# Performance work log

Hardware: AMD Instinct MI355X
Metric: run time of the kernel (lower is better)

Reference implementation:

```python
import jax, jax.numpy as jnp
import numpy as np

PAD = 1
ORDERS = ['back', 'down', 'front', 'left', 'right', 'top']
# connected face for each of ['up','down','left','right'] sides (from self.relation)
NEIGHBORS = {
    'back':  ['top', 'down', 'right', 'left'],
    'down':  ['front', 'back', 'left', 'right'],
    'front': ['top', 'down', 'left', 'right'],
    'left':  ['top', 'down', 'back', 'front'],
    'right': ['top', 'down', 'front', 'back'],
    'top':   ['back', 'front', 'left', 'right'],
}
SIDES = ['up', 'down', 'left', 'right']

def _rot_y(t):
    c, s = np.cos(t), np.sin(t)
    return np.array([[c, 0, s], [0, 1, 0], [-s, 0, c]], np.float64)

def _rot_x(t):
    c, s = np.cos(t), np.sin(t)
    return np.array([[1, 0, 0], [0, c, -s], [0, s, c]], np.float64)

def _precompute(h, pad):
    # Reconstruction of Equirec2Cube geometry used by SpherePad._GetLoc.
    # Padded cube face has side Wp = h + 2*pad and FOV theta = 2*arctan((0.5h+pad)/(0.5h)).
    Wp = h + 2 * pad
    cxp = (Wp - 1) / 2.0
    tan_half = (0.5 * h + pad) / (0.5 * h)  # tan(theta/2)
    fp = cxp / tan_half                      # focal of padded cube (pixel-edge convention)
    u = (np.arange(Wp) - cxp) / fp
    gx, gy = np.meshgrid(u, u)              # x right, y down, camera looks along +z
    grid = np.stack([gx, gy, np.ones_like(gx)], axis=-1)  # [Wp, Wp, 3] front-face rays
    # world->camera rotations per face, ordered/named to match ORDERS
    R = {'back': _rot_y(np.pi), 'down': _rot_x(np.pi / 2), 'front': np.eye(3),
         'left': _rot_y(np.pi / 2), 'right': _rot_y(-np.pi / 2), 'top': _rot_x(-np.pi / 2)}
    data = {}
    for face in ORDERS:
        data[face] = {}
        for j, side in enumerate(SIDES):
            conn = NEIGHBORS[face][j]
            Rrel = R[conn] @ R[face].T       # self-cam -> connected-cam
            g = grid @ Rrel.T                # [Wp, Wp, 3]
            # original FOV=90 K has f == cx, so normalized grid_sample coord = X/Z, Y/Z
            x = g[..., 0] / g[..., 2]
            y = g[..., 1] / g[..., 2]
            mask = (x >= -1.01) & (x <= 1.01) & (y >= -1.01) & (y <= 1.01)
            xy = np.clip(np.stack([x, y], axis=-1), -1.0, 1.0).astype(np.float32)
            if side == 'up':
                sl = (slice(0, pad), slice(None))
            elif side == 'down':
                sl = (slice(Wp - pad, Wp), slice(None))
            elif side == 'left':
                sl = (slice(None), slice(0, pad))
            else:
                sl = (slice(None), slice(Wp - pad, Wp))
            data[face][side] = (xy[sl], mask[sl])
    return data

def _grid_sample(img, grid):
    # img [N,C,H,W], grid [N,Hg,Wg,2] in [-1,1]; bilinear, align_corners=True
    N, C, H, W = img.shape
    x = (grid[..., 0] + 1.0) * 0.5 * (W - 1)
    y = (grid[..., 1] + 1.0) * 0.5 * (H - 1)
    x0 = jnp.floor(x)
    y0 = jnp.floor(y)
    wx = (x - x0)[..., None]
    wy = (y - y0)[..., None]
    x0i = jnp.clip(x0.astype(jnp.int32), 0, W - 1)
    x1i = jnp.clip(x0i + 1, 0, W - 1)
    y0i = jnp.clip(y0.astype(jnp.int32), 0, H - 1)
    y1i = jnp.clip(y0i + 1, 0, H - 1)
    b = jnp.arange(N)[:, None, None]
    v00 = img[b, :, y0i, x0i]  # [N,Hg,Wg,C]
    v01 = img[b, :, y0i, x1i]
    v10 = img[b, :, y1i, x0i]
    v11 = img[b, :, y1i, x1i]
    out = (v00 * (1 - wx) * (1 - wy) + v01 * wx * (1 - wy)
           + v10 * (1 - wx) * wy + v11 * wx * wy)
    return out.transpose(0, 3, 1, 2)  # [N,C,Hg,Wg]

def _forward(inputs, pad):
    bs, c, h, w = inputs.shape
    rep = bs // 6
    data = _precompute(h, pad)       # numpy constants, computed at trace time
    faces = inputs.reshape(rep, 6, c, h, w)   # inputs[i::6] == faces[:, i]
    outs = []
    for i, face in enumerate(ORDERS):
        tf = jnp.pad(faces[:, i], ((0, 0), (0, 0), (pad, pad), (pad, pad)))
        for j, side in enumerate(SIDES):
            conn = faces[:, ORDERS.index(NEIGHBORS[face][j])]
            xy, mask = data[face][side]
            grid = jnp.broadcast_to(jnp.asarray(xy), (rep,) + xy.shape)
            interp = _grid_sample(conn, grid)          # [rep,c,strip_h,strip_w]
            m = jnp.asarray(mask)[None, None]
            if side == 'up':
                tf = tf.at[:, :, :pad, :].set(jnp.where(m, interp, tf[:, :, :pad, :]))
            elif side == 'down':
                tf = tf.at[:, :, -pad:, :].set(jnp.where(m, interp, tf[:, :, -pad:, :]))
            elif side == 'left':
                tf = tf.at[:, :, :, :pad].set(jnp.where(m, interp, tf[:, :, :, :pad]))
            else:
                tf = tf.at[:, :, :, -pad:].set(jnp.where(m, interp, tf[:, :, :, -pad:]))
        outs.append(tf)
    # torch: cat by face then re-interleave -> out[k*6+i] = face i of panorama k
    return jnp.stack(outs, axis=1).reshape(bs, c, h + 2 * pad, w + 2 * pad)

def setup_inputs() -> dict:
    key = jax.random.key(0)
    inputs = jax.random.normal(key, (24, 256, 128, 128), dtype=jnp.float32)
    return {'inputs': inputs}

def reference(inputs):
    return _forward(inputs, PAD)
```

## Files before the change

kernel.cpp:

```cpp
#include <hip/hip_runtime.h>

#define H    128
#define WP   130
#define BPF  516
#define TBLN 3096

__constant__ int c_R[6][9] = {
  {-1,0,0,  0,1,0,  0,0,-1},
  { 1,0,0,  0,0,-1, 0,1,0 },
  { 1,0,0,  0,1,0,  0,0,1 },
  { 0,0,1,  0,1,0, -1,0,0 },
  { 0,0,-1, 0,1,0,  1,0,0 },
  { 1,0,0,  0,0,1,  0,-1,0},
};
__constant__ int c_conn[6][4] = {
  {5,1,4,3}, {2,0,3,4}, {5,1,3,4}, {5,1,0,2}, {5,1,2,0}, {0,2,3,4},
};

#define INV_FP (65.0f / 4128.0f)

__global__ void __launch_bounds__(256)
border_table_kernel(int* __restrict__ tb_face, int4* __restrict__ tb_idx,
                    float4* __restrict__ tb_w) {
  int t = blockIdx.x * 256 + threadIdx.x;
  if (t >= TBLN) return;
  int face = t / BPF;
  int k    = t - face * BPF;

  int r, c;
  if (k < 130)      { r = 0;        c = k; }
  else if (k < 260) { r = WP - 1;   c = k - 130; }
  else if (k < 388) { r = k - 259;  c = 0; }
  else              { r = k - 387;  c = WP - 1; }

  int fs = -1;
  int4  idx = make_int4(0, 0, 0, 0);
  float4 w  = make_float4(0.f, 0.f, 0.f, 0.f);

  int cand[2]; int nc = 0;
  if (c == WP - 1) cand[nc++] = 3;
  if (c == 0)      cand[nc++] = 2;
  if (r == WP - 1) cand[nc++] = 1;
  if (r == 0)      cand[nc++] = 0;

  float uc = ((float)c - 64.5f) * INV_FP;
  float ur = ((float)r - 64.5f) * INV_FP;

  for (int kk = 0; kk < nc; ++kk) {
    int s  = cand[kk];
    int cf = c_conn[face][s];
    const int* Rc = c_R[cf];
    const int* Rf = c_R[face];
    float g[3];
    #pragma unroll
    for (int i = 0; i < 3; ++i) {
      float acc = 0.0f;
      #pragma unroll
      for (int j = 0; j < 3; ++j) {
        int rr = Rc[i*3+0]*Rf[j*3+0] + Rc[i*3+1]*Rf[j*3+1] + Rc[i*3+2]*Rf[j*3+2];
        float dj = (j == 0) ? uc : (j == 1) ? ur : 1.0f;
        acc += (float)rr * dj;
      }
      g[i] = acc;
    }
    float x = g[0] / g[2];
    float y = g[1] / g[2];
    if (fabsf(x) <= 1.01f && fabsf(y) <= 1.01f) {
      x = fminf(fmaxf(x, -1.0f), 1.0f);
      y = fminf(fmaxf(y, -1.0f), 1.0f);
      float xp = (x + 1.0f) * 0.5f * (float)(H - 1);
      float yp = (y + 1.0f) * 0.5f * (float)(H - 1);
      float x0 = floorf(xp), y0 = floorf(yp);
      float wx = xp - x0,    wy = yp - y0;
      int x0i = min(max((int)x0, 0), H - 1);
      int x1i = min(x0i + 1, H - 1);
      int y0i = min(max((int)y0, 0), H - 1);
      int y1i = min(y0i + 1, H - 1);
      fs  = cf;
      idx = make_int4(y0i * H + x0i, y0i * H + x1i, y1i * H + x0i, y1i * H + x1i);
      w   = make_float4((1.f - wx) * (1.f - wy), wx * (1.f - wy),
                        (1.f - wx) * wy,         wx * wy);
      break;
    }
  }
  tb_face[t] = fs;
  tb_idx[t]  = idx;
  tb_w[t]    = w;
}

__global__ void __launch_bounds__(256)
fused_kernel(const float* __restrict__ in, float4* __restrict__ out4,
             const int* __restrict__ tb_face,
             const int4* __restrict__ tb_idx,
             const float4* __restrict__ tb_w) {
  const unsigned bx  = blockIdx.x;
  const unsigned img = blockIdx.y;
  const unsigned u   = threadIdx.x;

  if (bx < 16u) {
    unsigned hh = (bx << 3) + (u >> 5);
    unsigned l  = u & 31u;
    unsigned g  = hh + 1u;
    unsigned m  = g >> 1;
    unsigned h  = g & 1u;

    const float4* base = (const float4*)in + ((size_t)img << 12);
    float4 A = base[(hh << 5) + l];
    float bx0 = __shfl_down(A.x, 1, 32);
    float by0 = __shfl_down(A.y, 1, 32);
    float bz0 = __shfl_down(A.z, 1, 32);

    float4 o = h ? make_float4(A.y, A.z, A.w, bx0)
                 : make_float4(A.w, bx0, by0, bz0);
    if (l < 31u)
      out4[(size_t)img * 4225u + 65u * m + 1u + (h << 5) + l] = o;
  } else {
    unsigned n    = img >> 8;
    unsigned ch   = img & 255u;
    unsigned rep  = n / 6u;
    unsigned face = n - rep * 6u;

    for (unsigned k = u; k < 257u; k += 256u) {
      unsigned qk;
      if (k < 33u)       qk = k;
      else if (k == 33u) qk = 64u;
      else if (k == 34u) qk = 4160u;
      else if (k < 68u)  qk = 4192u + (k - 35u);
      else {
        unsigned jj = k - 68u;
        unsigned mm = 1u + jj / 3u;
        unsigned w  = jj - 3u * (jj / 3u);
        qk = 65u * mm + ((w == 0u) ? 0u : (w == 1u) ? 32u : 64u);
      }

      unsigned p = qk << 2;
      unsigned r = p / 130u;
      unsigned c = p - r * 130u;
      float vals[4];
      #pragma unroll
      for (int jj = 0; jj < 4; ++jj) {
        float v;
        if ((r - 1u) < 128u && (c - 1u) < 128u) {
          v = in[(img << 14) + ((r - 1u) << 7) + (c - 1u)];
        } else {
          unsigned tk = (r == 0u)   ? c
                      : (r == 129u) ? (130u + c)
                      : (c == 0u)   ? (259u + r)
                      :               (387u + r);
          unsigned ti = face * (unsigned)BPF + tk;
          int fs = tb_face[ti];
          v = 0.0f;
          if (fs >= 0) {
            int4   id = tb_idx[ti];
            float4 w  = tb_w[ti];
            const float* s = in +
                ((size_t)(((rep * 6u + (unsigned)fs) << 8) + ch) << 14);
            v = w.x * s[id.x] + w.y * s[id.y] + w.z * s[id.z] + w.w * s[id.w];
          }
        }
        vals[jj] = v;
        if (++c == 130u) { c = 0u; ++r; }
      }
      out4[(size_t)img * 4225u + qk] =
          make_float4(vals[0], vals[1], vals[2], vals[3]);
    }
  }
}

__global__ void __launch_bounds__(256)
interior_kernel(const float4* __restrict__ in4, float* __restrict__ out) {
  unsigned t = blockIdx.x * 256u + threadIdx.x;
  unsigned c4  = t & 31u;
  unsigned r   = (t >> 5) & 127u;
  unsigned img = t >> 12;
  float4 v = in4[t];
  unsigned o = img * 16900u + (r + 1u) * 130u + 1u + (c4 << 2);
  out[o] = v.x; out[o + 1] = v.y; out[o + 2] = v.z; out[o + 3] = v.w;
}

__global__ void __launch_bounds__(256)
border_kernel(const float* __restrict__ in, float* __restrict__ out) {
  unsigned tid = blockIdx.x * 256u + threadIdx.x;
  const unsigned total = 6144u * 516u;
  if (tid >= total) return;
  unsigned img = tid / 516u;
  unsigned k   = tid - img * 516u;
  int r, c;
  if (k < 130u)      { r = 0;               c = (int)k; }
  else if (k < 260u) { r = WP - 1;          c = (int)(k - 130u); }
  else if (k < 388u) { r = (int)(k - 259u); c = 0; }
  else               { r = (int)(k - 387u); c = WP - 1; }
  int n = (int)(img >> 8), ch = (int)(img & 255u);
  int face = n % 6, rep = n / 6;
  float v = 0.0f;
  int cand[2]; int nc = 0;
  if (c == WP - 1) cand[nc++] = 3;
  if (c == 0)      cand[nc++] = 2;
  if (r == WP - 1) cand[nc++] = 1;
  if (r == 0)      cand[nc++] = 0;
  float uc = ((float)c - 64.5f) * INV_FP;
  float ur = ((float)r - 64.5f) * INV_FP;
  for (int kk = 0; kk < nc; ++kk) {
    int s = cand[kk], cf = c_conn[face][s];
    const int* Rc = c_R[cf]; const int* Rf = c_R[face];
    float g[3];
    #pragma unroll
    for (int i = 0; i < 3; ++i) {
      float acc = 0.0f;
      #pragma unroll
      for (int j = 0; j < 3; ++j) {
        int rr = Rc[i*3+0]*Rf[j*3+0] + Rc[i*3+1]*Rf[j*3+1] + Rc[i*3+2]*Rf[j*3+2];
        float dj = (j == 0) ? uc : (j == 1) ? ur : 1.0f;
        acc += (float)rr * dj;
      }
      g[i] = acc;
    }
    float x = g[0] / g[2], y = g[1] / g[2];
    if (fabsf(x) <= 1.01f && fabsf(y) <= 1.01f) {
      x = fminf(fmaxf(x, -1.0f), 1.0f);
      y = fminf(fmaxf(y, -1.0f), 1.0f);
      const float* src = in + ((size_t)((rep * 6 + cf) * 256 + ch)) * H * H;
      float xp = (x + 1.0f) * 0.5f * (float)(H - 1);
      float yp = (y + 1.0f) * 0.5f * (float)(H - 1);
      float x0 = floorf(xp), y0 = floorf(yp);
      float wx = xp - x0, wy = yp - y0;
      int x0i = min(max((int)x0, 0), H - 1);
      int x1i = min(x0i + 1, H - 1);
      int y0i = min(max((int)y0, 0), H - 1);
      int y1i = min(y0i + 1, H - 1);
      v = src[y0i*H+x0i]*(1.f-wx)*(1.f-wy) + src[y0i*H+x1i]*wx*(1.f-wy)
        + src[y1i*H+x0i]*(1.f-wx)*wy       + src[y1i*H+x1i]*wx*wy;
      break;
    }
  }
  out[(unsigned)img * 16900u + (unsigned)r * 130u + (unsigned)c] = v;
}

extern "C" void kernel_launch(void* const* d_in, const int* in_sizes, int n_in,
                              void* d_out, int out_size, void* d_ws, size_t ws_size,
                              hipStream_t stream) {
  (void)in_sizes; (void)n_in; (void)out_size;
  const float* in = (const float*)d_in[0];
  float* out = (float*)d_out;

  const size_t need = (size_t)TBLN * (4 + 16 + 16);
  if (d_ws != nullptr && ws_size >= need) {
    int*    tb_face = (int*)d_ws;
    int4*   tb_idx  = (int4*)(tb_face + TBLN);
    float4* tb_w    = (float4*)(tb_idx + TBLN);
    border_table_kernel<<<(TBLN + 255) / 256, 256, 0, stream>>>(tb_face, tb_idx, tb_w);

    dim3 grid(17, 6144);
    fused_kernel<<<grid, 256, 0, stream>>>(in, (float4*)out,
                                           tb_face, tb_idx, tb_w);
  } else {
    interior_kernel<<<98304, 256, 0, stream>>>((const float4*)in, out);
    const unsigned btotal = 6144u * 516u;
    border_kernel<<<(btotal + 255u) / 256u, 256, 0, stream>>>(in, out);
  }
}
```

Baseline: 240.8 us.

## Stage image edge rows/columns in workspace so border pass reads compact buffer

The bulk copy kernel now also writes each image's first/last two rows and first/last four columns into a compact per-image staging buffer in workspace. A separate edge kernel then computes the border strips and bilinear samples from this staged data, using precomputed staged indices, instead of gathering scattered values from the full input. This aims to turn strided, poorly coalesced border gathers into reads from a small contiguous region. In exchange it adds an extra kernel launch, a dependency between the two passes, and about 37 MB of staging writes and reads.

```diff
diff --git a/kernel.cpp b/kernel.cpp
--- a/kernel.cpp
+++ b/kernel.cpp
@@ -4,6 +4,7 @@
 #define WP   130
 #define BPF  516
 #define TBLN 3096
+#define SPI  1536
 
 __constant__ int c_R[6][9] = {
   {-1,0,0,  0,1,0,  0,0,-1},
@@ -19,9 +20,16 @@
 
 #define INV_FP (65.0f / 4128.0f)
 
-__global__ void __launch_bounds__(256)
-border_table_kernel(int* __restrict__ tb_face, int4* __restrict__ tb_idx,
-                    float4* __restrict__ tb_w) {
+__device__ __forceinline__ int stage_index(int y, int x) {
+  if (x <= 3)   return 512 + y * 8 + x;
+  if (x >= 124) return 512 + y * 8 + 4 + (x - 124);
+  int slot = (y == 0) ? 0 : (y == 1) ? 1 : (y == 126) ? 2 : 3;
+  return slot * 128 + x;
+}
+
+__global__ void __launch_bounds__(256)
+border_table_kernel(int* __restrict__ tb_face, int4* __restrict__ tb_raw,
+                    int4* __restrict__ tb_stg, float4* __restrict__ tb_w) {
   int t = blockIdx.x * 256 + threadIdx.x;
   if (t >= TBLN) return;
   int face = t / BPF;
@@ -34,7 +42,8 @@
   else              { r = k - 387;  c = WP - 1; }
 
   int fs = -1;
-  int4  idx = make_int4(0, 0, 0, 0);
+  int4  raw = make_int4(0, 0, 0, 0);
+  int4  stg = make_int4(0, 0, 0, 0);
   float4 w  = make_float4(0.f, 0.f, 0.f, 0.f);
 
   int cand[2]; int nc = 0;
@@ -77,15 +86,113 @@
       int y0i = min(max((int)y0, 0), H - 1);
       int y1i = min(y0i + 1, H - 1);
       fs  = cf;
-      idx = make_int4(y0i * H + x0i, y0i * H + x1i, y1i * H + x0i, y1i * H + x1i);
+      raw = make_int4(y0i * H + x0i, y0i * H + x1i, y1i * H + x0i, y1i * H + x1i);
+      stg = make_int4(stage_index(y0i, x0i), stage_index(y0i, x1i),
+                      stage_index(y1i, x0i), stage_index(y1i, x1i));
       w   = make_float4((1.f - wx) * (1.f - wy), wx * (1.f - wy),
                         (1.f - wx) * wy,         wx * wy);
       break;
     }
   }
   tb_face[t] = fs;
-  tb_idx[t]  = idx;
+  tb_raw[t]  = raw;
+  tb_stg[t]  = stg;
   tb_w[t]    = w;
+}
+
+__global__ void __launch_bounds__(256)
+bulk_stage_kernel(const float* __restrict__ in, float4* __restrict__ out4,
+                  float* __restrict__ stage) {
+  const unsigned bx  = blockIdx.x;
+  const unsigned img = blockIdx.y;
+  const unsigned u   = threadIdx.x;
+
+  unsigned hh = (bx << 3) + (u >> 5);
+  unsigned l  = u & 31u;
+  unsigned g  = hh + 1u;
+  unsigned m  = g >> 1;
+  unsigned h  = g & 1u;
+
+  const float4* base = (const float4*)in + ((size_t)img << 12);
+  float4 A = base[(hh << 5) + l];
+  float bx0 = __shfl_down(A.x, 1, 32);
+  float by0 = __shfl_down(A.y, 1, 32);
+  float bz0 = __shfl_down(A.z, 1, 32);
+
+  float4 o = h ? make_float4(A.y, A.z, A.w, bx0)
+               : make_float4(A.w, bx0, by0, bz0);
+  if (l < 31u)
+    out4[(size_t)img * 4225u + 65u * m + 1u + (h << 5) + l] = o;
+
+  float* simg = stage + (size_t)img * SPI;
+  if (l == 0u)  *(float4*)(simg + 512u + hh * 8u)      = A;
+  if (l == 31u) *(float4*)(simg + 512u + hh * 8u + 4u) = A;
+  if (hh == 0u || hh == 1u || hh == 126u || hh == 127u) {
+    unsigned slot = (hh == 0u) ? 0u : (hh == 1u) ? 1u : (hh == 126u) ? 2u : 3u;
+    *(float4*)(simg + slot * 128u + (l << 2)) = A;
+  }
+}
+
+__global__ void __launch_bounds__(256)
+edge_stage_kernel(float4* __restrict__ out4, const float* __restrict__ stage,
+                  const int* __restrict__ tb_face,
+                  const int4* __restrict__ tb_stg,
+                  const float4* __restrict__ tb_w) {
+  const unsigned img = blockIdx.x;
+  const unsigned u   = threadIdx.x;
+
+  unsigned n    = img >> 8;
+  unsigned ch   = img & 255u;
+  unsigned rep  = n / 6u;
+  unsigned face = n - rep * 6u;
+  const float* simg = stage + (size_t)img * SPI;
+
+  for (unsigned k = u; k < 257u; k += 256u) {
+    unsigned qk;
+    if (k < 33u)       qk = k;
+    else if (k == 33u) qk = 64u;
+    else if (k == 34u) qk = 4160u;
+    else if (k < 68u)  qk = 4192u + (k - 35u);
+    else {
+      unsigned jj = k - 68u;
+      unsigned mm = 1u + jj / 3u;
+      unsigned w  = jj - 3u * (jj / 3u);
+      qk = 65u * mm + ((w == 0u) ? 0u : (w == 1u) ? 32u : 64u);
+    }
+
+    unsigned p = qk << 2;
+    unsigned r = p / 130u;
+    unsigned c = p - r * 130u;
+    float vals[4];
+    #pragma unroll
+    for (int jj = 0; jj < 4; ++jj) {
+      float v;
+      if ((r - 1u) < 128u && (c - 1u) < 128u) {
+        unsigned cc = c - 1u;
+        unsigned cs = (cc < 4u) ? cc : (cc - 120u);
+        v = simg[512u + (r - 1u) * 8u + cs];
+      } else {
+        unsigned tk = (r == 0u)   ? c
+                    : (r == 129u) ? (130u + c)
+                    : (c == 0u)   ? (259u + r)
+                    :               (387u + r);
+        unsigned ti = face * (unsigned)BPF + tk;
+        int fs = tb_face[ti];
+        v = 0.0f;
+        if (fs >= 0) {
+          int4   id = tb_stg[ti];
+          float4 w  = tb_w[ti];
+          const float* sj = stage +
+              (size_t)(((rep * 6u + (unsigned)fs) << 8) + ch) * SPI;
+          v = w.x * sj[id.x] + w.y * sj[id.y] + w.z * sj[id.z] + w.w * sj[id.w];
+        }
+      }
+      vals[jj] = v;
+      if (++c == 130u) { c = 0u; ++r; }
+    }
+    out4[(size_t)img * 4225u + qk] =
+        make_float4(vals[0], vals[1], vals[2], vals[3]);
+  }
 }
 
 __global__ void __launch_bounds__(256)
@@ -243,16 +350,28 @@
   const float* in = (const float*)d_in[0];
   float* out = (float*)d_out;
 
-  const size_t need = (size_t)TBLN * (4 + 16 + 16);
-  if (d_ws != nullptr && ws_size >= need) {
+  const size_t tbl_bytes  = (size_t)TBLN * (4 + 16 + 16 + 16);
+  const size_t need_full  = tbl_bytes + (size_t)6144 * SPI * 4;
+
+  if (d_ws != nullptr && ws_size >= tbl_bytes) {
     int*    tb_face = (int*)d_ws;
-    int4*   tb_idx  = (int4*)(tb_face + TBLN);
-    float4* tb_w    = (float4*)(tb_idx + TBLN);
-    border_table_kernel<<<(TBLN + 255) / 256, 256, 0, stream>>>(tb_face, tb_idx, tb_w);
-
-    dim3 grid(17, 6144);
-    fused_kernel<<<grid, 256, 0, stream>>>(in, (float4*)out,
-                                           tb_face, tb_idx, tb_w);
+    int4*   tb_raw  = (int4*)(tb_face + TBLN);
+    int4*   tb_stg  = tb_raw + TBLN;
+    float4* tb_w    = (float4*)(tb_stg + TBLN);
+    border_table_kernel<<<(TBLN + 255) / 256, 256, 0, stream>>>(
+        tb_face, tb_raw, tb_stg, tb_w);
+
+    if (ws_size >= need_full) {
+      float* stage = (float*)(tb_w + TBLN);
+      dim3 gridB(16, 6144);
+      bulk_stage_kernel<<<gridB, 256, 0, stream>>>(in, (float4*)out, stage);
+      edge_stage_kernel<<<6144, 256, 0, stream>>>((float4*)out, stage,
+                                                  tb_face, tb_stg, tb_w);
+    } else {
+      dim3 grid(17, 6144);
+      fused_kernel<<<grid, 256, 0, stream>>>(in, (float4*)out,
+                                             tb_face, tb_raw, tb_w);
+    }
   } else {
     interior_kernel<<<98304, 256, 0, stream>>>((const float4*)in, out);
     const unsigned btotal = 6144u * 516u;
```

Result: slower. 248.0 us (+3.0%).

## Restructure padding copy into one 1024-thread block per image plus border block

Applied to the files above, without the earlier changes.

Replaces the 17-blocks-per-image layout with two 1024-thread blocks per image. One block copies the whole interior using four float4 items per thread, loading two adjacent float4s directly instead of shuffling across lanes. The other block fills the border with one thread per output float4. This cuts block count and shuffle work, but leaves most threads of the border block idle and may reduce scheduling flexibility with the larger blocks.

```diff
diff --git a/kernel.cpp b/kernel.cpp
--- a/kernel.cpp
+++ b/kernel.cpp
@@ -4,6 +4,7 @@
 #define WP   130
 #define BPF  516
 #define TBLN 3096
+#define NIMG 6144
 
 __constant__ int c_R[6][9] = {
   {-1,0,0,  0,1,0,  0,0,-1},
@@ -88,82 +89,95 @@
   tb_w[t]    = w;
 }
 
-__global__ void __launch_bounds__(256)
-fused_kernel(const float* __restrict__ in, float4* __restrict__ out4,
-             const int* __restrict__ tb_face,
-             const int4* __restrict__ tb_idx,
-             const float4* __restrict__ tb_w) {
-  const unsigned bx  = blockIdx.x;
+__global__ void __launch_bounds__(1024)
+mlp_kernel(const float* __restrict__ in, float4* __restrict__ out4,
+           const int* __restrict__ tb_face,
+           const int4* __restrict__ tb_idx,
+           const float4* __restrict__ tb_w) {
   const unsigned img = blockIdx.y;
-  const unsigned u   = threadIdx.x;
-
-  if (bx < 16u) {
-    unsigned hh = (bx << 3) + (u >> 5);
-    unsigned l  = u & 31u;
-    unsigned g  = hh + 1u;
-    unsigned m  = g >> 1;
-    unsigned h  = g & 1u;
-
-    const float4* base = (const float4*)in + ((size_t)img << 12);
-    float4 A = base[(hh << 5) + l];
-    float bx0 = __shfl_down(A.x, 1, 32);
-    float by0 = __shfl_down(A.y, 1, 32);
-    float bz0 = __shfl_down(A.z, 1, 32);
-
-    float4 o = h ? make_float4(A.y, A.z, A.w, bx0)
-                 : make_float4(A.w, bx0, by0, bz0);
-    if (l < 31u)
-      out4[(size_t)img * 4225u + 65u * m + 1u + (h << 5) + l] = o;
+
+  if (blockIdx.x == 0u) {
+    const unsigned u = threadIdx.x;
+    const float4* bin = (const float4*)in + ((size_t)img << 12);
+
+    float4 A[4], B[4];
+    unsigned oq[4], od[4];
+    bool act[4];
+    #pragma unroll
+    for (int k = 0; k < 4; ++k) {
+      unsigned tau = u + ((unsigned)k << 10);
+      act[k] = (tau < 3968u);
+      unsigned tt = act[k] ? tau : 0u;
+      unsigned j  = tt / 62u;
+      unsigned i  = tt - j * 62u;
+      unsigned m  = (j == 0u && i < 31u) ? 64u : j;
+      unsigned o  = (i >= 31u) ? 1u : 0u;
+      unsigned q  = i + 1u + o;
+      unsigned ib = (m << 6) + q - 33u;
+      A[k] = bin[ib];
+      B[k] = bin[ib + 1u];
+      oq[k] = m * 65u + q;
+      od[k] = o;
+    }
+    const size_t ob = (size_t)img * 4225u;
+    #pragma unroll
+    for (int k = 0; k < 4; ++k) {
+      if (!act[k]) continue;
+      float4 o = od[k] ? make_float4(A[k].y, A[k].z, A[k].w, B[k].x)
+                       : make_float4(A[k].w, B[k].x, B[k].y, B[k].z);
+      out4[ob + oq[k]] = o;
+    }
   } else {
+    const unsigned k = threadIdx.x;
+    if (k >= 257u) return;
+
     unsigned n    = img >> 8;
     unsigned ch   = img & 255u;
     unsigned rep  = n / 6u;
     unsigned face = n - rep * 6u;
 
-    for (unsigned k = u; k < 257u; k += 256u) {
-      unsigned qk;
-      if (k < 33u)       qk = k;
-      else if (k == 33u) qk = 64u;
-      else if (k == 34u) qk = 4160u;
-      else if (k < 68u)  qk = 4192u + (k - 35u);
-      else {
-        unsigned jj = k - 68u;
-        unsigned mm = 1u + jj / 3u;
-        unsigned w  = jj - 3u * (jj / 3u);
-        qk = 65u * mm + ((w == 0u) ? 0u : (w == 1u) ? 32u : 64u);
+    unsigned qk;
+    if (k < 33u)       qk = k;
+    else if (k == 33u) qk = 64u;
+    else if (k == 34u) qk = 4160u;
+    else if (k < 68u)  qk = 4192u + (k - 35u);
+    else {
+      unsigned jj = k - 68u;
+      unsigned mm = 1u + jj / 3u;
+      unsigned w  = jj - 3u * (jj / 3u);
+      qk = 65u * mm + ((w == 0u) ? 0u : (w == 1u) ? 32u : 64u);
+    }
+
+    unsigned p = qk << 2;
+    unsigned r = p / 130u;
+    unsigned c = p - r * 130u;
+    float vals[4];
+    #pragma unroll
+    for (int e = 0; e < 4; ++e) {
+      float v;
+      if ((r - 1u) < 128u && (c - 1u) < 128u) {
+        v = in[((size_t)img << 14) + ((r - 1u) << 7) + (c - 1u)];
+      } else {
+        unsigned tk = (r == 0u)   ? c
+                    : (r == 129u) ? (130u + c)
+                    : (c == 0u)   ? (259u + r)
+                    :               (387u + r);
+        unsigned ti = face * (unsigned)BPF + tk;
+        int fs = tb_face[ti];
+        v = 0.0f;
+        if (fs >= 0) {
+          int4   id = tb_idx[ti];
+          float4 w  = tb_w[ti];
+          const float* s = in +
+              ((size_t)(((rep * 6u + (unsigned)fs) << 8) + ch) << 14);
+          v = w.x * s[id.x] + w.y * s[id.y] + w.z * s[id.z] + w.w * s[id.w];
+        }
       }
-
-      unsigned p = qk << 2;
-      unsigned r = p / 130u;
-      unsigned c = p - r * 130u;
-      float vals[4];
-      #pragma unroll
-      for (int jj = 0; jj < 4; ++jj) {
-        float v;
-        if ((r - 1u) < 128u && (c - 1u) < 128u) {
-          v = in[(img << 14) + ((r - 1u) << 7) + (c - 1u)];
-        } else {
-          unsigned tk = (r == 0u)   ? c
-                      : (r == 129u) ? (130u + c)
-                      : (c == 0u)   ? (259u + r)
-                      :               (387u + r);
-          unsigned ti = face * (unsigned)BPF + tk;
-          int fs = tb_face[ti];
-          v = 0.0f;
-          if (fs >= 0) {
-            int4   id = tb_idx[ti];
-            float4 w  = tb_w[ti];
-            const float* s = in +
-                ((size_t)(((rep * 6u + (unsigned)fs) << 8) + ch) << 14);
-            v = w.x * s[id.x] + w.y * s[id.y] + w.z * s[id.z] + w.w * s[id.w];
-          }
-        }
-        vals[jj] = v;
-        if (++c == 130u) { c = 0u; ++r; }
-      }
-      out4[(size_t)img * 4225u + qk] =
-          make_float4(vals[0], vals[1], vals[2], vals[3]);
-    }
+      vals[e] = v;
+      if (++c == 130u) { c = 0u; ++r; }
+    }
+    out4[(size_t)img * 4225u + qk] =
+        make_float4(vals[0], vals[1], vals[2], vals[3]);
   }
 }
 
@@ -243,16 +257,18 @@
   const float* in = (const float*)d_in[0];
   float* out = (float*)d_out;
 
-  const size_t need = (size_t)TBLN * (4 + 16 + 16);
-  if (d_ws != nullptr && ws_size >= need) {
+  const size_t tbl_bytes = (size_t)TBLN * (4 + 16 + 16);
+
+  if (d_ws != nullptr && ws_size >= tbl_bytes) {
     int*    tb_face = (int*)d_ws;
     int4*   tb_idx  = (int4*)(tb_face + TBLN);
     float4* tb_w    = (float4*)(tb_idx + TBLN);
-    border_table_kernel<<<(TBLN + 255) / 256, 256, 0, stream>>>(tb_face, tb_idx, tb_w);
-
-    dim3 grid(17, 6144);
-    fused_kernel<<<grid, 256, 0, stream>>>(in, (float4*)out,
-                                           tb_face, tb_idx, tb_w);
+    border_table_kernel<<<(TBLN + 255) / 256, 256, 0, stream>>>(
+        tb_face, tb_idx, tb_w);
+
+    dim3 grid(2, NIMG);
+    mlp_kernel<<<grid, 1024, 0, stream>>>(in, (float4*)out,
+                                          tb_face, tb_idx, tb_w);
   } else {
     interior_kernel<<<98304, 256, 0, stream>>>((const float4*)in, out);
     const unsigned btotal = 6144u * 516u;
```

After: 251.6 us. 4.5% more time.
